# Kernel optimization log

Measured on AMD Instinct MI355X. Metric: run time of the kernel, lower is better.

## Reference

```python
import jax, jax.numpy as jnp
import numpy as np

EPS = 1e-5

def _bn(x, g, b, m, v):
    # inference-mode BatchNorm over channel axis 1
    shp = [1] * x.ndim
    shp[1] = x.shape[1]
    return (x - m.reshape(shp)) * (g.reshape(shp) / jnp.sqrt(v.reshape(shp) + EPS)) + b.reshape(shp)

def _forward(x, wdr, bdr, g1, be1, m1, v1, g2, be2, m2, v2, wrow, brow, wfc, bfc,
             wdrs, bdrs, g3, be3, m3, v3, g4, be4, m4, v4, wrows, brows, wfcs, bfcs):
    B, C, H, W = x.shape
    r = jax.nn.relu(x)

    # ---- channel attention (chan_att) ----
    y = jnp.einsum('bchw,oc->bohw', r, wdr) + bdr[None, :, None, None]   # 1x1 conv DR
    y = jax.nn.relu(_bn(y, g1, be1, m1, v1))
    Bc, D, _, _ = y.shape
    M = H * W
    yf = y.reshape(B, D, M)
    yc = yf - yf.mean(axis=2, keepdims=True)
    cov = jnp.einsum('bcm,bdm->bcd', yc, yc) / M                         # MPNCOV CovpoolLayer: x I_hat x^T, [B,D,D]
    cov = _bn(cov, g2, be2, m2, v2)                                      # row_bn (channel axis = D)
    # grouped conv: per-channel i, 4 filters over row i -> [B, D, 4]
    vch = jnp.einsum('bik,ijk->bij', cov, wrow).reshape(B, -1) + brow    # [B, 4D]
    catt = jax.nn.sigmoid(vch @ wfc.T + bfc)                             # fc_adapt_channels -> [B, C]
    catt = catt[:, :, None, None]

    # ---- spatial attention (pos_att) ----
    s = jnp.einsum('bchw,oc->bohw', r, wdrs) + bdrs[None, :, None, None]
    s = _bn(s, g3, be3, m3, v3)
    fh, fw = H // 8, W // 8
    sp = s.reshape(B, D, 8, fh, 8, fw).mean(axis=(3, 5))                 # adaptive avg pool -> 8x8
    M2 = 64
    sf = sp.reshape(B, D, M2)
    # cov_feature: x^T I_hat x with I_hat = (1/M2)(I_D - (1/M2) J_D)
    colsum = sf.sum(axis=1)                                              # [B, 64]
    covs = (jnp.einsum('bcm,bcn->bmn', sf, sf)
            - colsum[:, :, None] * colsum[:, None, :] / M2) / M2         # [B,64,64]
    covs = _bn(covs, g4, be4, m4, v4)
    vs = jnp.einsum('bik,ijk->bij', covs, wrows).reshape(B, -1) + brows  # [B,256]
    vs = jax.nn.relu(vs)
    patt = jax.nn.sigmoid(vs @ wfcs.T + bfcs)                            # [B,64]
    patt = patt.reshape(B, 1, 8, 8)
    patt = jnp.repeat(jnp.repeat(patt, fh, axis=2), fw, axis=3)          # adaptive unpool (exact replication)

    # attention == '+'
    return x * catt + jax.nn.relu(x * patt)

def setup_inputs() -> dict:
    key = jax.random.key(0)
    ks = jax.random.split(key, 32)
    B, C, H, W, D = 32, 512, 56, 56, 128
    n = lambda k, s, sc: jax.random.normal(k, s, dtype=jnp.float32) * sc
    u = lambda k, s: jax.random.uniform(k, s, dtype=jnp.float32)
    inp = {
        'x': n(ks[0], (B, C, H, W), 1.0),
        'wdr': n(ks[1], (D, C), 0.04), 'bdr': n(ks[2], (D,), 0.02),
        'g1': u(ks[3], (D,)) + 0.5, 'be1': n(ks[4], (D,), 0.1), 'm1': n(ks[5], (D,), 0.1), 'v1': u(ks[6], (D,)) * 0.5 + 0.5,
        'g2': u(ks[7], (D,)) + 0.5, 'be2': n(ks[8], (D,), 0.1), 'm2': n(ks[9], (D,), 0.1), 'v2': u(ks[10], (D,)) * 0.5 + 0.5,
        'wrow': n(ks[11], (D, 4, D), 0.08), 'brow': n(ks[12], (4 * D,), 0.02),
        'wfc': n(ks[13], (C, 4 * D), 0.04), 'bfc': n(ks[14], (C,), 0.02),
        'wdrs': n(ks[15], (D, C), 0.04), 'bdrs': n(ks[16], (D,), 0.02),
        'g3': u(ks[17], (D,)) + 0.5, 'be3': n(ks[18], (D,), 0.1), 'm3': n(ks[19], (D,), 0.1), 'v3': u(ks[20], (D,)) * 0.5 + 0.5,
        'g4': u(ks[21], (64,)) + 0.5, 'be4': n(ks[22], (64,), 0.1), 'm4': n(ks[23], (64,), 0.1), 'v4': u(ks[24], (64,)) * 0.5 + 0.5,
        'wrows': n(ks[25], (64, 4, 64), 0.1), 'brows': n(ks[26], (256,), 0.02),
        'wfcs': n(ks[27], (64, 256), 0.06), 'bfcs': n(ks[28], (64,), 0.02),
    }
    return inp

def reference(x, wdr, bdr, g1, be1, m1, v1, g2, be2, m2, v2, wrow, brow, wfc, bfc,
              wdrs, bdrs, g3, be3, m3, v3, g4, be4, m4, v4, wrows, brows, wfcs, bfcs):
    return _forward(x, wdr, bdr, g1, be1, m1, v1, g2, be2, m2, v2, wrow, brow, wfc, bfc,
                    wdrs, bdrs, g3, be3, m3, v3, g4, be4, m4, v4, wrows, brows, wfcs, bfcs)
```

## Files before the change

### kernel.cpp

```cpp
#include <hip/hip_runtime.h>
#include <hip/hip_bf16.h>

#define EPS 1e-5f

typedef short bf16x8 __attribute__((ext_vector_type(8)));
typedef float f32x4  __attribute__((ext_vector_type(4)));

union BF8 { ushort u[8]; bf16x8 v; };

__device__ __forceinline__ ushort f2bf(float f) {
  uint u = __float_as_uint(f);
  u += 0x7fffu + ((u >> 16) & 1u);
  return (ushort)(u >> 16);
}
__device__ __forceinline__ float bf2f(ushort u) {
  return __uint_as_float(((uint)u) << 16);
}
__device__ __forceinline__ f32x4 mfma16(bf16x8 a, bf16x8 b, f32x4 c) {
  return __builtin_amdgcn_mfma_f32_16x16x32_bf16(a, b, c, 0, 0, 0);
}

__global__ __launch_bounds__(256) void k_zero(float4* __restrict__ p) {
  p[blockIdx.x * 256 + threadIdx.x] = make_float4(0.f, 0.f, 0.f, 0.f);
}

__global__ __launch_bounds__(256) void k_prep(
    const float* __restrict__ wdr, const float* __restrict__ wdrs,
    const float* __restrict__ bdr,
    const float* __restrict__ g1, const float* __restrict__ be1,
    const float* __restrict__ m1, const float* __restrict__ v1,
    const float* __restrict__ wfc,
    ushort* __restrict__ wdr_bf, ushort* __restrict__ wdrs_bf,
    float* __restrict__ sc1, float* __restrict__ sh1,
    float* __restrict__ wfcT) {
  int i = blockIdx.x * 256 + threadIdx.x;
  if (i < 65536) {
    wdr_bf[i]  = f2bf(wdr[i]);
    wdrs_bf[i] = f2bf(wdrs[i] * (1.0f / 49.0f));
  }
  if (i < 262144) {
    int c = i >> 9, p = i & 511;
    wfcT[p * 512 + c] = wfc[i];
  }
  if (i < 128) {
    float a = g1[i] / sqrtf(v1[i] + EPS);
    sc1[i] = a;
    sh1[i] = (bdr[i] - m1[i]) * a + be1[i];
  }
}

__global__ __launch_bounds__(256) void k_convy(
    const float* __restrict__ x, const ushort* __restrict__ wdr_bf,
    const float* __restrict__ sc1, const float* __restrict__ sh1,
    ushort* __restrict__ y_bf, float* __restrict__ rp) {
  __shared__ ushort xs[2][9216];
  __shared__ float pool[2][1024];
  __shared__ float sc_s[128], sh_s[128];

  const int t  = threadIdx.x;
  const int b  = blockIdx.y;
  const int n0 = blockIdx.x * 128;

  if (t < 128) { sc_s[t] = sc1[t]; sh_s[t] = sh1[t]; }
#pragma unroll
  for (int f = 0; f < 4; f++) { pool[0][t + f * 256] = 0.f; pool[1][t + f * 256] = 0.f; }

  const int cl = t & 7;
  const int nq = t >> 3;
  const int nl = nq * 4;
  const int ng = n0 + nl;
  const bool nv = ng < 3136;
  const int h   = ng / 56;
  const int w   = ng - h * 56;
  const int gh0 = (n0 / 56) / 7;
  const int lb0 = (h / 7 - gh0) * 8 + (w / 7);
  const int lb3 = (h / 7 - gh0) * 8 + ((w + 3) / 7);
  int split = 7 - (w % 7); if (split > 4) split = 4;
  const int ng8  = nq >> 1;
  const int nsub = (nq & 1) * 4;

  const int l  = t & 63;
  const int wv = t >> 6;
  const int wr = wv >> 1, wc = wv & 1;
  const int lm = l & 15,  lk = l >> 4;

  const float* xb = x + (size_t)(b * 512) * 3136 + ng;

  f32x4 acc[4][4];
#pragma unroll
  for (int a = 0; a < 4; a++)
#pragma unroll
    for (int c = 0; c < 4; c++) acc[a][c] = (f32x4){0.f, 0.f, 0.f, 0.f};

  const float4 z4 = make_float4(0.f, 0.f, 0.f, 0.f);
  float4 rA[8], rB[8];

#pragma unroll
  for (int r = 0; r < 8; r++) {
    rA[r] = z4;
    if (nv) rA[r] = *(const float4*)(xb + (size_t)(r * 8 + cl) * 3136);
  }

  __syncthreads();

  for (int kc = 0; kc < 8; kc++) {
    if (kc < 7) {
#pragma unroll
      for (int r = 0; r < 8; r++) {
        rB[r] = z4;
        if (nv) rB[r] = *(const float4*)(xb + (size_t)((kc + 1) * 64 + r * 8 + cl) * 3136);
      }
    }

    ushort* xsb = xs[kc & 1];
    float*  plb = pool[kc & 1];
#pragma unroll
    for (int r = 0; r < 8; r++) {
      int cc = r * 8 + cl;
      float e0 = fmaxf(rA[r].x, 0.f), e1 = fmaxf(rA[r].y, 0.f);
      float e2 = fmaxf(rA[r].z, 0.f), e3 = fmaxf(rA[r].w, 0.f);
      if (nv) {
        float s0 = e0, s1 = 0.f;
        if (split > 1) s0 += e1; else s1 += e1;
        if (split > 2) s0 += e2; else s1 += e2;
        if (split > 3) s0 += e3; else s1 += e3;
        atomicAdd(&plb[cc * 16 + lb0], s0);
        if (lb3 != lb0) atomicAdd(&plb[cc * 16 + lb3], s1);
      }
      int base = (cc >> 3) * 1152 + ng8 * 72 + nsub * 8 + (cc & 7);
      xsb[base]      = f2bf(e0);
      xsb[base + 8]  = f2bf(e1);
      xsb[base + 16] = f2bf(e2);
      xsb[base + 24] = f2bf(e3);
    }
    __syncthreads();

#pragma unroll
    for (int ki = 0; ki < 2; ki++) {
      bf16x8 af[4], bfr[4];
#pragma unroll
      for (int mi = 0; mi < 4; mi++) {
        int m = wr * 64 + mi * 16 + lm;
        af[mi] = *(const bf16x8*)(wdr_bf + m * 512 + kc * 64 + ki * 32 + lk * 8);
      }
#pragma unroll
      for (int ni = 0; ni < 4; ni++) {
        int n = wc * 64 + ni * 16 + lm;
        int a = (ki * 4 + lk) * 1152 + (n >> 3) * 72 + (n & 7) * 8;
        bfr[ni] = *(const bf16x8*)(xsb + a);
      }
#pragma unroll
      for (int mi = 0; mi < 4; mi++)
#pragma unroll
        for (int ni = 0; ni < 4; ni++)
          acc[mi][ni] = mfma16(af[mi], bfr[ni], acc[mi][ni]);
    }

#pragma unroll
    for (int f = 0; f < 4; f++) {
      int idx = t + f * 256;
      float pv = plb[idx];
      int cL = idx >> 4, lb = idx & 15;
      int gbin = gh0 * 8 + lb;
      if (pv != 0.f && gbin < 64)
        atomicAdd(&rp[((size_t)(b * 64 + gbin)) * 512 + kc * 64 + cL], pv);
      plb[idx] = 0.f;
    }

    if (kc < 7) {
#pragma unroll
      for (int r = 0; r < 8; r++) rA[r] = rB[r];
    }
  }

#pragma unroll
  for (int mi = 0; mi < 4; mi++) {
#pragma unroll
    for (int ni = 0; ni < 4; ni++) {
      int n_g = n0 + wc * 64 + ni * 16 + lm;
      if (n_g >= 3136) continue;
#pragma unroll
      for (int r = 0; r < 4; r++) {
        int m = wr * 64 + mi * 16 + lk * 4 + r;
        float v = acc[mi][ni][r] * sc_s[m] + sh_s[m];
        v = fmaxf(v, 0.f);
        y_bf[((size_t)(b * 128 + m)) * 3136 + n_g] = f2bf(v);
      }
    }
  }
}

__global__ __launch_bounds__(256) void k_gram(
    const ushort* __restrict__ y_bf, float* __restrict__ G, float* __restrict__ S) {
  __shared__ ushort ys[2][128 * 40];
  const int t  = threadIdx.x;
  const int b  = blockIdx.y;
  const int k0 = blockIdx.x * 448;

  const int l  = t & 63, wv = t >> 6;
  const int wr = wv >> 1, wc = wv & 1;
  const int lm = l & 15,  lk = l >> 4;

  const int mA = t >> 2, k8 = t & 3;
  const ushort* yb = y_bf + ((size_t)(b * 128 + mA)) * 3136 + k0 + k8 * 8;
  const size_t rowoff = (size_t)64 * 3136;

  f32x4 acc[4][4];
#pragma unroll
  for (int a = 0; a < 4; a++)
#pragma unroll
    for (int c = 0; c < 4; c++) acc[a][c] = (f32x4){0.f, 0.f, 0.f, 0.f};
  float sA = 0.f, sB = 0.f;

  BF8 a0, a1, b0, b1;
  a0.v = *(const bf16x8*)(yb);
  a1.v = *(const bf16x8*)(yb + rowoff);

  for (int kc = 0; kc < 14; kc++) {
    if (kc < 13) {
      b0.v = *(const bf16x8*)(yb + (kc + 1) * 32);
      b1.v = *(const bf16x8*)(yb + rowoff + (kc + 1) * 32);
    }
#pragma unroll
    for (int j = 0; j < 8; j++) { sA += bf2f(a0.u[j]); sB += bf2f(a1.u[j]); }
    ushort* ysb = ys[kc & 1];
    *(bf16x8*)(ysb + mA * 40 + k8 * 8) = a0.v;
    *(bf16x8*)(ysb + (mA + 64) * 40 + k8 * 8) = a1.v;
    __syncthreads();

    bf16x8 af[4], bfr[4];
#pragma unroll
    for (int mi = 0; mi < 4; mi++)
      af[mi] = *(const bf16x8*)(ysb + (wr * 64 + mi * 16 + lm) * 40 + lk * 8);
#pragma unroll
    for (int ni = 0; ni < 4; ni++)
      bfr[ni] = *(const bf16x8*)(ysb + (wc * 64 + ni * 16 + lm) * 40 + lk * 8);
#pragma unroll
    for (int mi = 0; mi < 4; mi++)
#pragma unroll
      for (int ni = 0; ni < 4; ni++)
        acc[mi][ni] = mfma16(af[mi], bfr[ni], acc[mi][ni]);

    if (kc < 13) { a0 = b0; a1 = b1; }
  }

#pragma unroll
  for (int mi = 0; mi < 4; mi++)
#pragma unroll
    for (int ni = 0; ni < 4; ni++)
#pragma unroll
      for (int r = 0; r < 4; r++) {
        int i = wr * 64 + mi * 16 + lk * 4 + r;
        int j = wc * 64 + ni * 16 + lm;
        atomicAdd(&G[((size_t)(b * 128 + i)) * 128 + j], acc[mi][ni][r]);
      }
  atomicAdd(&S[b * 128 + mA], sA);
  atomicAdd(&S[b * 128 + mA + 64], sB);
}

__global__ __launch_bounds__(256) void k_catt(
    const float* __restrict__ G, const float* __restrict__ S,
    const float* __restrict__ g2, const float* __restrict__ be2,
    const float* __restrict__ m2, const float* __restrict__ v2,
    const float* __restrict__ wrow, const float* __restrict__ brow,
    const float* __restrict__ wfcT, const float* __restrict__ bfc,
    float* __restrict__ catt) {
  __shared__ float Ss[128];
  __shared__ float vch_s[512];
  const int t = threadIdx.x;
  const int b = blockIdx.x;
  const float invM = 1.0f / 3136.0f;
  if (t < 128) Ss[t] = S[b * 128 + t];
  __syncthreads();
#pragma unroll
  for (int rep = 0; rep < 2; rep++) {
    int p = t + rep * 256;
    int i = p >> 2, j = p & 3;
    float a2  = g2[i] / sqrtf(v2[i] + EPS);
    float mi2 = m2[i], bei = be2[i];
    float Si  = Ss[i] * invM;
    const float* Grow = G + ((size_t)(b * 128 + i)) * 128;
    const float* wr_  = wrow + (i * 4 + j) * 128;
    float a = 0.f;
    for (int k = 0; k < 128; k++) {
      float cov = (Grow[k] - Si * Ss[k]) * invM;
      a += ((cov - mi2) * a2 + bei) * wr_[k];
    }
    vch_s[p] = a + brow[p];
  }
  __syncthreads();
#pragma unroll
  for (int rep = 0; rep < 2; rep++) {
    int c = t + rep * 256;
    float z = bfc[c];
    for (int p = 0; p < 512; p++) z += vch_s[p] * wfcT[p * 512 + c];
    catt[b * 512 + c] = 1.f / (1.f + expf(-z));
  }
}

__global__ __launch_bounds__(256) void k_sconv(
    const float* __restrict__ rp, const ushort* __restrict__ wdrs_bf,
    const float* __restrict__ bdrs,
    const float* __restrict__ g3, const float* __restrict__ be3,
    const float* __restrict__ m3, const float* __restrict__ v3,
    ushort* __restrict__ sfT) {
  const int t = threadIdx.x;
  const int b = blockIdx.x;
  const int l = t & 63, wv = t >> 6;
  const int wm = wv >> 1, wn = wv & 1;
  const int lm = l & 15,  lk = l >> 4;
  f32x4 acc[4][2];
#pragma unroll
  for (int a = 0; a < 4; a++) { acc[a][0] = (f32x4){0.f,0.f,0.f,0.f}; acc[a][1] = (f32x4){0.f,0.f,0.f,0.f}; }

  for (int kk = 0; kk < 16; kk++) {
    bf16x8 af[4], bfr[2];
#pragma unroll
    for (int mi = 0; mi < 4; mi++) {
      int m = wm * 64 + mi * 16 + lm;
      af[mi] = *(const bf16x8*)(wdrs_bf + m * 512 + kk * 32 + lk * 8);
    }
#pragma unroll
    for (int ni = 0; ni < 2; ni++) {
      int g = wn * 32 + ni * 16 + lm;
      const float* pb = rp + ((size_t)(b * 64 + g)) * 512 + kk * 32 + lk * 8;
      float4 fa = *(const float4*)pb;
      float4 fb = *(const float4*)(pb + 4);
      BF8 bb;
      bb.u[0] = f2bf(fa.x); bb.u[1] = f2bf(fa.y); bb.u[2] = f2bf(fa.z); bb.u[3] = f2bf(fa.w);
      bb.u[4] = f2bf(fb.x); bb.u[5] = f2bf(fb.y); bb.u[6] = f2bf(fb.z); bb.u[7] = f2bf(fb.w);
      bfr[ni] = bb.v;
    }
#pragma unroll
    for (int mi = 0; mi < 4; mi++)
#pragma unroll
      for (int ni = 0; ni < 2; ni++)
        acc[mi][ni] = mfma16(af[mi], bfr[ni], acc[mi][ni]);
  }
#pragma unroll
  for (int mi = 0; mi < 4; mi++)
#pragma unroll
    for (int ni = 0; ni < 2; ni++) {
      int g = wn * 32 + ni * 16 + lm;
#pragma unroll
      for (int r = 0; r < 4; r++) {
        int d = wm * 64 + mi * 16 + lk * 4 + r;
        float a3 = g3[d] / sqrtf(v3[d] + EPS);
        float sf = (acc[mi][ni][r] + bdrs[d] - m3[d]) * a3 + be3[d];
        sfT[((size_t)(b * 64 + g)) * 128 + d] = f2bf(sf);
      }
    }
}

__global__ __launch_bounds__(256) void k_patt(
    const ushort* __restrict__ sfT,
    const float* __restrict__ g4, const float* __restrict__ be4,
    const float* __restrict__ m4, const float* __restrict__ v4,
    const float* __restrict__ wrows, const float* __restrict__ brows,
    const float* __restrict__ wfcs, const float* __restrict__ bfcs,
    float* __restrict__ patt) {
  __shared__ float colsum_s[64];
  __shared__ float covbn_s[64 * 65];
  __shared__ float vs_s[256];
  const int t = threadIdx.x;
  const int b = blockIdx.x;
  if (t < 64) {
    float cs = 0.f;
    const ushort* row = sfT + ((size_t)(b * 64 + t)) * 128;
    for (int dq = 0; dq < 16; dq++) {
      BF8 v; v.v = *(const bf16x8*)(row + dq * 8);
#pragma unroll
      for (int j = 0; j < 8; j++) cs += bf2f(v.u[j]);
    }
    colsum_s[t] = cs;
  }
  __syncthreads();

  const int l = t & 63, wv = t >> 6;
  const int wr = wv >> 1, wc = wv & 1;
  const int lm = l & 15,  lk = l >> 4;
  f32x4 acc[2][2];
  acc[0][0] = (f32x4){0.f,0.f,0.f,0.f}; acc[0][1] = (f32x4){0.f,0.f,0.f,0.f};
  acc[1][0] = (f32x4){0.f,0.f,0.f,0.f}; acc[1][1] = (f32x4){0.f,0.f,0.f,0.f};
  for (int kk = 0; kk < 4; kk++) {
    bf16x8 af[2], bfr[2];
#pragma unroll
    for (int mi = 0; mi < 2; mi++)
      af[mi] = *(const bf16x8*)(sfT + ((size_t)(b * 64 + wr * 32 + mi * 16 + lm)) * 128 + kk * 32 + lk * 8);
#pragma unroll
    for (int ni = 0; ni < 2; ni++)
      bfr[ni] = *(const bf16x8*)(sfT + ((size_t)(b * 64 + wc * 32 + ni * 16 + lm)) * 128 + kk * 32 + lk * 8);
#pragma unroll
    for (int mi = 0; mi < 2; mi++)
#pragma unroll
      for (int ni = 0; ni < 2; ni++)
        acc[mi][ni] = mfma16(af[mi], bfr[ni], acc[mi][ni]);
  }
  const float inv64 = 1.0f / 64.0f;
#pragma unroll
  for (int mi = 0; mi < 2; mi++)
#pragma unroll
    for (int ni = 0; ni < 2; ni++) {
      int j = wc * 32 + ni * 16 + lm;
#pragma unroll
      for (int r = 0; r < 4; r++) {
        int i = wr * 32 + mi * 16 + lk * 4 + r;
        float cv = (acc[mi][ni][r] - colsum_s[i] * colsum_s[j] * inv64) * inv64;
        float a4 = g4[i] / sqrtf(v4[i] + EPS);
        covbn_s[i * 65 + j] = (cv - m4[i]) * a4 + be4[i];
      }
    }
  __syncthreads();
  {
    int m = t >> 2, j = t & 3;
    float a = brows[t];
    const float* wr_ = wrows + (m * 4 + j) * 64;
    for (int k = 0; k < 64; k++) a += covbn_s[m * 65 + k] * wr_[k];
    vs_s[t] = fmaxf(a, 0.f);
  }
  __syncthreads();
  if (t < 64) {
    float z = bfcs[t];
    const float* wf = wfcs + t * 256;
    for (int p = 0; p < 256; p++) z += vs_s[p] * wf[p];
    patt[b * 64 + t] = 1.f / (1.f + expf(-z));
  }
}

__global__ __launch_bounds__(256) void k_final(
    const float* __restrict__ x, const float* __restrict__ catt,
    const float* __restrict__ patt, float* __restrict__ out) {
  int gi = blockIdx.x * 256 + threadIdx.x;
  int bc = gi / 784;
  int q  = gi - bc * 784;
  int n  = q * 4;
  int b  = bc >> 9;
  float ca = catt[bc];
  int h = n / 56;
  int w = n - h * 56;
  const float* pp = patt + b * 64 + (h / 7) * 8;
  float p0 = pp[w / 7], p1 = pp[(w + 1) / 7], p2 = pp[(w + 2) / 7], p3 = pp[(w + 3) / 7];
  float4 xv = *(const float4*)(x + (size_t)gi * 4);
  float4 o;
  o.x = xv.x * ca + fmaxf(xv.x * p0, 0.f);
  o.y = xv.y * ca + fmaxf(xv.y * p1, 0.f);
  o.z = xv.z * ca + fmaxf(xv.z * p2, 0.f);
  o.w = xv.w * ca + fmaxf(xv.w * p3, 0.f);
  *(float4*)(out + (size_t)gi * 4) = o;
}

extern "C" void kernel_launch(void* const* d_in, const int* in_sizes, int n_in,
                              void* d_out, int out_size, void* d_ws, size_t ws_size,
                              hipStream_t stream) {
  const float* x     = (const float*)d_in[0];
  const float* wdr   = (const float*)d_in[1];
  const float* bdr   = (const float*)d_in[2];
  const float* g1    = (const float*)d_in[3];
  const float* be1   = (const float*)d_in[4];
  const float* m1    = (const float*)d_in[5];
  const float* v1    = (const float*)d_in[6];
  const float* g2    = (const float*)d_in[7];
  const float* be2   = (const float*)d_in[8];
  const float* m2    = (const float*)d_in[9];
  const float* v2    = (const float*)d_in[10];
  const float* wrow  = (const float*)d_in[11];
  const float* brow  = (const float*)d_in[12];
  const float* wfc   = (const float*)d_in[13];
  const float* bfc   = (const float*)d_in[14];
  const float* wdrs  = (const float*)d_in[15];
  const float* bdrs  = (const float*)d_in[16];
  const float* g3    = (const float*)d_in[17];
  const float* be3   = (const float*)d_in[18];
  const float* m3    = (const float*)d_in[19];
  const float* v3    = (const float*)d_in[20];
  const float* g4    = (const float*)d_in[21];
  const float* be4   = (const float*)d_in[22];
  const float* m4    = (const float*)d_in[23];
  const float* v4    = (const float*)d_in[24];
  const float* wrows = (const float*)d_in[25];
  const float* brows = (const float*)d_in[26];
  const float* wfcs  = (const float*)d_in[27];
  const float* bfcs  = (const float*)d_in[28];

  char* ob = (char*)d_out;
  ushort* y_bf    = (ushort*)(ob + 0x0000000);
  ushort* wdr_bf  = (ushort*)(ob + 0x2000000);
  ushort* wdrs_bf = (ushort*)(ob + 0x2020000);
  float*  sc1     = (float*) (ob + 0x2040000);
  float*  sh1     = (float*) (ob + 0x2040200);
  float*  wfcT    = (float*) (ob + 0x2050000);
  float*  rp      = (float*) (ob + 0x2150000);
  float*  G       = (float*) (ob + 0x2550000);
  float*  S       = (float*) (ob + 0x2750000);
  ushort* sfT     = (ushort*)(ob + 0x2760000);

  char* ws = (char*)d_ws;
  float* catt = (float*)(ws + 0x00000);
  float* patt = (float*)(ws + 0x10000);

  k_zero<<<1540, 256, 0, stream>>>((float4*)(ob + 0x2150000));

  k_prep<<<1024, 256, 0, stream>>>(wdr, wdrs, bdr, g1, be1, m1, v1, wfc,
                                   wdr_bf, wdrs_bf, sc1, sh1, wfcT);
  k_convy<<<dim3(25, 32), 256, 0, stream>>>(x, wdr_bf, sc1, sh1, y_bf, rp);
  k_gram<<<dim3(7, 32), 256, 0, stream>>>(y_bf, G, S);
  k_catt<<<32, 256, 0, stream>>>(G, S, g2, be2, m2, v2, wrow, brow, wfcT, bfc, catt);
  k_sconv<<<32, 256, 0, stream>>>(rp, wdrs_bf, bdrs, g3, be3, m3, v3, sfT);
  k_patt<<<32, 256, 0, stream>>>(sfT, g4, be4, m4, v4, wrows, brows, wfcs, bfcs, patt);
  k_final<<<50176, 256, 0, stream>>>(x, catt, patt, (float*)d_out);
}
```

Before: 633.0 us.

## Fuse zeroing into prep, merge tail kernels, unroll-by-two with ping-pong registers

Folds the zeroing kernel into k_prep by widening its grid, and merges k_catt, k_sconv and k_patt into one k_tail kernel that keeps the spatial feature matrix in LDS instead of global memory. In k_convy and k_gram the K loops are unrolled by two with swapped register buffers to remove the prefetch copies. Plain __syncthreads is replaced with an explicit LDS wait plus barrier, and the weight fragments in k_convy are hoisted before the barrier. This removes three kernel launches and a global round trip but serialises the channel and spatial tail work within 32 blocks.

```diff
diff --git a/kernel.cpp b/kernel.cpp
--- a/kernel.cpp
+++ b/kernel.cpp
@@ -20,8 +20,10 @@
   return __builtin_amdgcn_mfma_f32_16x16x32_bf16(a, b, c, 0, 0, 0);
 }
 
-__global__ __launch_bounds__(256) void k_zero(float4* __restrict__ p) {
-  p[blockIdx.x * 256 + threadIdx.x] = make_float4(0.f, 0.f, 0.f, 0.f);
+__device__ __forceinline__ void bar_lds() {
+  asm volatile("s_waitcnt lgkmcnt(0)" ::: "memory");
+  __builtin_amdgcn_s_barrier();
+  __builtin_amdgcn_sched_barrier(0);
 }
 
 __global__ __launch_bounds__(256) void k_prep(
@@ -32,8 +34,9 @@
     const float* __restrict__ wfc,
     ushort* __restrict__ wdr_bf, ushort* __restrict__ wdrs_bf,
     float* __restrict__ sc1, float* __restrict__ sh1,
-    float* __restrict__ wfcT) {
+    float* __restrict__ wfcT, float4* __restrict__ zdst) {
   int i = blockIdx.x * 256 + threadIdx.x;
+  zdst[i] = make_float4(0.f, 0.f, 0.f, 0.f);
   if (i < 65536) {
     wdr_bf[i]  = f2bf(wdr[i]);
     wdrs_bf[i] = f2bf(wdrs[i] * (1.0f / 49.0f));
@@ -103,22 +106,28 @@
 
   __syncthreads();
 
-  for (int kc = 0; kc < 8; kc++) {
+  auto body = [&](int kc, float4 (&cur)[8], float4 (&nxt)[8]) {
     if (kc < 7) {
 #pragma unroll
       for (int r = 0; r < 8; r++) {
-        rB[r] = z4;
-        if (nv) rB[r] = *(const float4*)(xb + (size_t)((kc + 1) * 64 + r * 8 + cl) * 3136);
-      }
-    }
+        nxt[r] = z4;
+        if (nv) nxt[r] = *(const float4*)(xb + (size_t)((kc + 1) * 64 + r * 8 + cl) * 3136);
+      }
+    }
+    bf16x8 af_[2][4];
+#pragma unroll
+    for (int ki = 0; ki < 2; ki++)
+#pragma unroll
+      for (int mi = 0; mi < 4; mi++)
+        af_[ki][mi] = *(const bf16x8*)(wdr_bf + (wr * 64 + mi * 16 + lm) * 512 + kc * 64 + ki * 32 + lk * 8);
 
     ushort* xsb = xs[kc & 1];
     float*  plb = pool[kc & 1];
 #pragma unroll
     for (int r = 0; r < 8; r++) {
       int cc = r * 8 + cl;
-      float e0 = fmaxf(rA[r].x, 0.f), e1 = fmaxf(rA[r].y, 0.f);
-      float e2 = fmaxf(rA[r].z, 0.f), e3 = fmaxf(rA[r].w, 0.f);
+      float e0 = fmaxf(cur[r].x, 0.f), e1 = fmaxf(cur[r].y, 0.f);
+      float e2 = fmaxf(cur[r].z, 0.f), e3 = fmaxf(cur[r].w, 0.f);
       if (nv) {
         float s0 = e0, s1 = 0.f;
         if (split > 1) s0 += e1; else s1 += e1;
@@ -133,16 +142,11 @@
       xsb[base + 16] = f2bf(e2);
       xsb[base + 24] = f2bf(e3);
     }
-    __syncthreads();
+    bar_lds();
 
 #pragma unroll
     for (int ki = 0; ki < 2; ki++) {
-      bf16x8 af[4], bfr[4];
-#pragma unroll
-      for (int mi = 0; mi < 4; mi++) {
-        int m = wr * 64 + mi * 16 + lm;
-        af[mi] = *(const bf16x8*)(wdr_bf + m * 512 + kc * 64 + ki * 32 + lk * 8);
-      }
+      bf16x8 bfr[4];
 #pragma unroll
       for (int ni = 0; ni < 4; ni++) {
         int n = wc * 64 + ni * 16 + lm;
@@ -153,7 +157,7 @@
       for (int mi = 0; mi < 4; mi++)
 #pragma unroll
         for (int ni = 0; ni < 4; ni++)
-          acc[mi][ni] = mfma16(af[mi], bfr[ni], acc[mi][ni]);
+          acc[mi][ni] = mfma16(af_[ki][mi], bfr[ni], acc[mi][ni]);
     }
 
 #pragma unroll
@@ -166,11 +170,11 @@
         atomicAdd(&rp[((size_t)(b * 64 + gbin)) * 512 + kc * 64 + cL], pv);
       plb[idx] = 0.f;
     }
-
-    if (kc < 7) {
-#pragma unroll
-      for (int r = 0; r < 8; r++) rA[r] = rB[r];
-    }
+  };
+
+  for (int kc2 = 0; kc2 < 8; kc2 += 2) {
+    body(kc2,     rA, rB);
+    body(kc2 + 1, rB, rA);
   }
 
 #pragma unroll
@@ -216,17 +220,17 @@
   a0.v = *(const bf16x8*)(yb);
   a1.v = *(const bf16x8*)(yb + rowoff);
 
-  for (int kc = 0; kc < 14; kc++) {
+  auto gbody = [&](int kc, BF8& c0, BF8& c1, BF8& n0_, BF8& n1_) {
     if (kc < 13) {
-      b0.v = *(const bf16x8*)(yb + (kc + 1) * 32);
-      b1.v = *(const bf16x8*)(yb + rowoff + (kc + 1) * 32);
-    }
-#pragma unroll
-    for (int j = 0; j < 8; j++) { sA += bf2f(a0.u[j]); sB += bf2f(a1.u[j]); }
+      n0_.v = *(const bf16x8*)(yb + (kc + 1) * 32);
+      n1_.v = *(const bf16x8*)(yb + rowoff + (kc + 1) * 32);
+    }
+#pragma unroll
+    for (int j = 0; j < 8; j++) { sA += bf2f(c0.u[j]); sB += bf2f(c1.u[j]); }
     ushort* ysb = ys[kc & 1];
-    *(bf16x8*)(ysb + mA * 40 + k8 * 8) = a0.v;
-    *(bf16x8*)(ysb + (mA + 64) * 40 + k8 * 8) = a1.v;
-    __syncthreads();
+    *(bf16x8*)(ysb + mA * 40 + k8 * 8) = c0.v;
+    *(bf16x8*)(ysb + (mA + 64) * 40 + k8 * 8) = c1.v;
+    bar_lds();
 
     bf16x8 af[4], bfr[4];
 #pragma unroll
@@ -240,8 +244,11 @@
 #pragma unroll
       for (int ni = 0; ni < 4; ni++)
         acc[mi][ni] = mfma16(af[mi], bfr[ni], acc[mi][ni]);
-
-    if (kc < 13) { a0 = b0; a1 = b1; }
+  };
+
+  for (int kc2 = 0; kc2 < 14; kc2 += 2) {
+    gbody(kc2,     a0, a1, b0, b1);
+    gbody(kc2 + 1, b0, b1, a0, a1);
   }
 
 #pragma unroll
@@ -258,17 +265,30 @@
   atomicAdd(&S[b * 128 + mA + 64], sB);
 }
 
-__global__ __launch_bounds__(256) void k_catt(
+__global__ __launch_bounds__(256) void k_tail(
     const float* __restrict__ G, const float* __restrict__ S,
     const float* __restrict__ g2, const float* __restrict__ be2,
     const float* __restrict__ m2, const float* __restrict__ v2,
     const float* __restrict__ wrow, const float* __restrict__ brow,
     const float* __restrict__ wfcT, const float* __restrict__ bfc,
-    float* __restrict__ catt) {
+    const float* __restrict__ rp, const ushort* __restrict__ wdrs_bf,
+    const float* __restrict__ bdrs,
+    const float* __restrict__ g3, const float* __restrict__ be3,
+    const float* __restrict__ m3, const float* __restrict__ v3,
+    const float* __restrict__ g4, const float* __restrict__ be4,
+    const float* __restrict__ m4, const float* __restrict__ v4,
+    const float* __restrict__ wrows, const float* __restrict__ brows,
+    const float* __restrict__ wfcs, const float* __restrict__ bfcs,
+    float* __restrict__ catt, float* __restrict__ patt) {
   __shared__ float Ss[128];
   __shared__ float vch_s[512];
+  __shared__ ushort sf_s[64 * 128];
+  __shared__ float colsum_s[64];
+  __shared__ float covbn_s[64 * 65];
+  __shared__ float vs_s[256];
   const int t = threadIdx.x;
   const int b = blockIdx.x;
+
   const float invM = 1.0f / 3136.0f;
   if (t < 128) Ss[t] = S[b * 128 + t];
   __syncthreads();
@@ -296,77 +316,58 @@
     for (int p = 0; p < 512; p++) z += vch_s[p] * wfcT[p * 512 + c];
     catt[b * 512 + c] = 1.f / (1.f + expf(-z));
   }
-}
-
-__global__ __launch_bounds__(256) void k_sconv(
-    const float* __restrict__ rp, const ushort* __restrict__ wdrs_bf,
-    const float* __restrict__ bdrs,
-    const float* __restrict__ g3, const float* __restrict__ be3,
-    const float* __restrict__ m3, const float* __restrict__ v3,
-    ushort* __restrict__ sfT) {
-  const int t = threadIdx.x;
-  const int b = blockIdx.x;
-  const int l = t & 63, wv = t >> 6;
-  const int wm = wv >> 1, wn = wv & 1;
-  const int lm = l & 15,  lk = l >> 4;
-  f32x4 acc[4][2];
-#pragma unroll
-  for (int a = 0; a < 4; a++) { acc[a][0] = (f32x4){0.f,0.f,0.f,0.f}; acc[a][1] = (f32x4){0.f,0.f,0.f,0.f}; }
-
-  for (int kk = 0; kk < 16; kk++) {
-    bf16x8 af[4], bfr[2];
-#pragma unroll
-    for (int mi = 0; mi < 4; mi++) {
-      int m = wm * 64 + mi * 16 + lm;
-      af[mi] = *(const bf16x8*)(wdrs_bf + m * 512 + kk * 32 + lk * 8);
-    }
-#pragma unroll
-    for (int ni = 0; ni < 2; ni++) {
-      int g = wn * 32 + ni * 16 + lm;
-      const float* pb = rp + ((size_t)(b * 64 + g)) * 512 + kk * 32 + lk * 8;
-      float4 fa = *(const float4*)pb;
-      float4 fb = *(const float4*)(pb + 4);
-      BF8 bb;
-      bb.u[0] = f2bf(fa.x); bb.u[1] = f2bf(fa.y); bb.u[2] = f2bf(fa.z); bb.u[3] = f2bf(fa.w);
-      bb.u[4] = f2bf(fb.x); bb.u[5] = f2bf(fb.y); bb.u[6] = f2bf(fb.z); bb.u[7] = f2bf(fb.w);
-      bfr[ni] = bb.v;
+
+  {
+    const int l = t & 63, wv = t >> 6;
+    const int wm = wv >> 1, wn = wv & 1;
+    const int lm = l & 15,  lk = l >> 4;
+    f32x4 acc[4][2];
+#pragma unroll
+    for (int a = 0; a < 4; a++) { acc[a][0] = (f32x4){0.f,0.f,0.f,0.f}; acc[a][1] = (f32x4){0.f,0.f,0.f,0.f}; }
+
+    for (int kk = 0; kk < 16; kk++) {
+      bf16x8 af[4], bfr[2];
+#pragma unroll
+      for (int mi = 0; mi < 4; mi++) {
+        int m = wm * 64 + mi * 16 + lm;
+        af[mi] = *(const bf16x8*)(wdrs_bf + m * 512 + kk * 32 + lk * 8);
+      }
+#pragma unroll
+      for (int ni = 0; ni < 2; ni++) {
+        int g = wn * 32 + ni * 16 + lm;
+        const float* pb = rp + ((size_t)(b * 64 + g)) * 512 + kk * 32 + lk * 8;
+        float4 fa = *(const float4*)pb;
+        float4 fb = *(const float4*)(pb + 4);
+        BF8 bb;
+        bb.u[0] = f2bf(fa.x); bb.u[1] = f2bf(fa.y); bb.u[2] = f2bf(fa.z); bb.u[3] = f2bf(fa.w);
+        bb.u[4] = f2bf(fb.x); bb.u[5] = f2bf(fb.y); bb.u[6] = f2bf(fb.z); bb.u[7] = f2bf(fb.w);
+        bfr[ni] = bb.v;
+      }
+#pragma unroll
+      for (int mi = 0; mi < 4; mi++)
+#pragma unroll
+        for (int ni = 0; ni < 2; ni++)
+          acc[mi][ni] = mfma16(af[mi], bfr[ni], acc[mi][ni]);
     }
 #pragma unroll
     for (int mi = 0; mi < 4; mi++)
 #pragma unroll
-      for (int ni = 0; ni < 2; ni++)
-        acc[mi][ni] = mfma16(af[mi], bfr[ni], acc[mi][ni]);
-  }
-#pragma unroll
-  for (int mi = 0; mi < 4; mi++)
-#pragma unroll
-    for (int ni = 0; ni < 2; ni++) {
-      int g = wn * 32 + ni * 16 + lm;
-#pragma unroll
-      for (int r = 0; r < 4; r++) {
-        int d = wm * 64 + mi * 16 + lk * 4 + r;
-        float a3 = g3[d] / sqrtf(v3[d] + EPS);
-        float sf = (acc[mi][ni][r] + bdrs[d] - m3[d]) * a3 + be3[d];
-        sfT[((size_t)(b * 64 + g)) * 128 + d] = f2bf(sf);
-      }
-    }
-}
-
-__global__ __launch_bounds__(256) void k_patt(
-    const ushort* __restrict__ sfT,
-    const float* __restrict__ g4, const float* __restrict__ be4,
-    const float* __restrict__ m4, const float* __restrict__ v4,
-    const float* __restrict__ wrows, const float* __restrict__ brows,
-    const float* __restrict__ wfcs, const float* __restrict__ bfcs,
-    float* __restrict__ patt) {
-  __shared__ float colsum_s[64];
-  __shared__ float covbn_s[64 * 65];
-  __shared__ float vs_s[256];
-  const int t = threadIdx.x;
-  const int b = blockIdx.x;
+      for (int ni = 0; ni < 2; ni++) {
+        int g = wn * 32 + ni * 16 + lm;
+#pragma unroll
+        for (int r = 0; r < 4; r++) {
+          int d = wm * 64 + mi * 16 + lk * 4 + r;
+          float a3 = g3[d] / sqrtf(v3[d] + EPS);
+          float sf = (acc[mi][ni][r] + bdrs[d] - m3[d]) * a3 + be3[d];
+          sf_s[g * 128 + d] = f2bf(sf);
+        }
+      }
+  }
+  __syncthreads();
+
   if (t < 64) {
     float cs = 0.f;
-    const ushort* row = sfT + ((size_t)(b * 64 + t)) * 128;
+    const ushort* row = sf_s + t * 128;
     for (int dq = 0; dq < 16; dq++) {
       BF8 v; v.v = *(const bf16x8*)(row + dq * 8);
 #pragma unroll
@@ -376,40 +377,42 @@
   }
   __syncthreads();
 
-  const int l = t & 63, wv = t >> 6;
-  const int wr = wv >> 1, wc = wv & 1;
-  const int lm = l & 15,  lk = l >> 4;
-  f32x4 acc[2][2];
-  acc[0][0] = (f32x4){0.f,0.f,0.f,0.f}; acc[0][1] = (f32x4){0.f,0.f,0.f,0.f};
-  acc[1][0] = (f32x4){0.f,0.f,0.f,0.f}; acc[1][1] = (f32x4){0.f,0.f,0.f,0.f};
-  for (int kk = 0; kk < 4; kk++) {
-    bf16x8 af[2], bfr[2];
+  {
+    const int l = t & 63, wv = t >> 6;
+    const int wr = wv >> 1, wc = wv & 1;
+    const int lm = l & 15,  lk = l >> 4;
+    f32x4 acc[2][2];
+    acc[0][0] = (f32x4){0.f,0.f,0.f,0.f}; acc[0][1] = (f32x4){0.f,0.f,0.f,0.f};
+    acc[1][0] = (f32x4){0.f,0.f,0.f,0.f}; acc[1][1] = (f32x4){0.f,0.f,0.f,0.f};
+    for (int kk = 0; kk < 4; kk++) {
+      bf16x8 af[2], bfr[2];
+#pragma unroll
+      for (int mi = 0; mi < 2; mi++)
+        af[mi] = *(const bf16x8*)(sf_s + (wr * 32 + mi * 16 + lm) * 128 + kk * 32 + lk * 8);
+#pragma unroll
+      for (int ni = 0; ni < 2; ni++)
+        bfr[ni] = *(const bf16x8*)(sf_s + (wc * 32 + ni * 16 + lm) * 128 + kk * 32 + lk * 8);
+#pragma unroll
+      for (int mi = 0; mi < 2; mi++)
+#pragma unroll
+        for (int ni = 0; ni < 2; ni++)
+          acc[mi][ni] = mfma16(af[mi], bfr[ni], acc[mi][ni]);
+    }
+    const float inv64 = 1.0f / 64.0f;
 #pragma unroll
     for (int mi = 0; mi < 2; mi++)
-      af[mi] = *(const bf16x8*)(sfT + ((size_t)(b * 64 + wr * 32 + mi * 16 + lm)) * 128 + kk * 32 + lk * 8);
-#pragma unroll
-    for (int ni = 0; ni < 2; ni++)
-      bfr[ni] = *(const bf16x8*)(sfT + ((size_t)(b * 64 + wc * 32 + ni * 16 + lm)) * 128 + kk * 32 + lk * 8);
-#pragma unroll
-    for (int mi = 0; mi < 2; mi++)
-#pragma unroll
-      for (int ni = 0; ni < 2; ni++)
-        acc[mi][ni] = mfma16(af[mi], bfr[ni], acc[mi][ni]);
-  }
-  const float inv64 = 1.0f / 64.0f;
-#pragma unroll
-  for (int mi = 0; mi < 2; mi++)
-#pragma unroll
-    for (int ni = 0; ni < 2; ni++) {
-      int j = wc * 32 + ni * 16 + lm;
-#pragma unroll
-      for (int r = 0; r < 4; r++) {
-        int i = wr * 32 + mi * 16 + lk * 4 + r;
-        float cv = (acc[mi][ni][r] - colsum_s[i] * colsum_s[j] * inv64) * inv64;
-        float a4 = g4[i] / sqrtf(v4[i] + EPS);
-        covbn_s[i * 65 + j] = (cv - m4[i]) * a4 + be4[i];
-      }
-    }
+#pragma unroll
+      for (int ni = 0; ni < 2; ni++) {
+        int j = wc * 32 + ni * 16 + lm;
+#pragma unroll
+        for (int r = 0; r < 4; r++) {
+          int i = wr * 32 + mi * 16 + lk * 4 + r;
+          float cv = (acc[mi][ni][r] - colsum_s[i] * colsum_s[j] * inv64) * inv64;
+          float a4 = g4[i] / sqrtf(v4[i] + EPS);
+          covbn_s[i * 65 + j] = (cv - m4[i]) * a4 + be4[i];
+        }
+      }
+  }
   __syncthreads();
   {
     int m = t >> 2, j = t & 3;
@@ -493,19 +496,20 @@
   float*  G       = (float*) (ob + 0x2550000);
   float*  S       = (float*) (ob + 0x2750000);
   ushort* sfT     = (ushort*)(ob + 0x2760000);
+  (void)sfT;
 
   char* ws = (char*)d_ws;
   float* catt = (float*)(ws + 0x00000);
   float* patt = (float*)(ws + 0x10000);
 
-  k_zero<<<1540, 256, 0, stream>>>((float4*)(ob + 0x2150000));
-
-  k_prep<<<1024, 256, 0, stream>>>(wdr, wdrs, bdr, g1, be1, m1, v1, wfc,
-                                   wdr_bf, wdrs_bf, sc1, sh1, wfcT);
+  k_prep<<<1540, 256, 0, stream>>>(wdr, wdrs, bdr, g1, be1, m1, v1, wfc,
+                                   wdr_bf, wdrs_bf, sc1, sh1, wfcT,
+                                   (float4*)(ob + 0x2150000));
   k_convy<<<dim3(25, 32), 256, 0, stream>>>(x, wdr_bf, sc1, sh1, y_bf, rp);
   k_gram<<<dim3(7, 32), 256, 0, stream>>>(y_bf, G, S);
-  k_catt<<<32, 256, 0, stream>>>(G, S, g2, be2, m2, v2, wrow, brow, wfcT, bfc, catt);
-  k_sconv<<<32, 256, 0, stream>>>(rp, wdrs_bf, bdrs, g3, be3, m3, v3, sfT);
-  k_patt<<<32, 256, 0, stream>>>(sfT, g4, be4, m4, v4, wrows, brows, wfcs, bfcs, patt);
+  k_tail<<<32, 256, 0, stream>>>(G, S, g2, be2, m2, v2, wrow, brow, wfcT, bfc,
+                                 rp, wdrs_bf, bdrs, g3, be3, m3, v3,
+                                 g4, be4, m4, v4, wrows, brows, wfcs, bfcs,
+                                 catt, patt);
   k_final<<<50176, 256, 0, stream>>>(x, catt, patt, (float*)d_out);
 }
```

Result: slower. 704.2 us (+11.2%).
